# Optimization experiments

Hardware: AMD Instinct MI355X
Metric: run time of the kernel (lower is better)

The kernel has to match this reference:

```python
import jax, jax.numpy as jnp
import numpy as np


def setup_inputs() -> dict:
    key = jax.random.key(0)
    kx, kw = jax.random.split(key)
    x = jax.random.normal(kx, (32, 64, 112, 112), dtype=jnp.float32)
    weights = jax.random.normal(kw, (128, 64, 3, 3), dtype=jnp.float32)
    return {"x": x, "weights": weights}


def reference(x, weights):
    # The torch module's triple loop computes a standard VALID conv2d,
    # stride 1, no padding, weights shared across spatial locations.
    # x: [B, Cin, H, W]; weights: [Cout, Cin, k, k] -> out: [B, Cout, H-k+1, W-k+1]
    out = jax.lax.conv_general_dilated(
        x, weights,
        window_strides=(1, 1),
        padding="VALID",
        dimension_numbers=("NCHW", "OIHW", "NCHW"),
    )
    return out
```

## Files before the change

### kernel.cpp

```cpp
#include <hip/hip_runtime.h>


typedef short bf16x8 __attribute__((ext_vector_type(8)));
typedef float f32x4 __attribute__((ext_vector_type(4)));

__device__ __forceinline__ unsigned short f2bf(float f) {
    unsigned int u = __builtin_bit_cast(unsigned int, f);
    unsigned int r = u + 0x7fffu + ((u >> 16) & 1u);
    return (unsigned short)(r >> 16);
}

__global__ void wperm_kernel(const float* __restrict__ W, unsigned short* __restrict__ wp) {
    int t = blockIdx.x * 256 + threadIdx.x;
    if (t < 73728) {
        int r  = t >> 13;
        int co = (t >> 6) & 127;
        int ci = t & 63;
        wp[t] = f2bf(W[(co * 64 + ci) * 9 + r]);
    }
}

__global__ __launch_bounds__(256, 2) void conv_mfma(const float* __restrict__ x,
                                                    const unsigned short* __restrict__ wp,
                                                    float* __restrict__ out) {
    __shared__ alignas(16) unsigned short xwin[324 * 72];
    __shared__ alignas(16) unsigned short wpl[128 * 72];

    const int tid  = threadIdx.x;
    const int lane = tid & 63;
    const int wv   = tid >> 6;
    const int quad = lane >> 4;
    const int l15  = lane & 15;

    const int b    = blockIdx.x / 49;
    const int tile = blockIdx.x % 49;
    const int oh0  = (tile / 7) * 16;
    const int ow0  = (tile % 7) * 16;

    const float* xb = x + b * 64 * 12544;
    for (int task = tid; task < 288; task += 256) {
        const int cg = task / 18;
        const int hh = task % 18;
        const int h  = min(oh0 + hh, 111);
        const float* xr = xb + (cg * 4) * 12544 + h * 112;
        unsigned short* dst = &xwin[(hh * 18) * 72 + cg * 4];
        #pragma unroll
        for (int ww = 0; ww < 18; ww++) {
            const int w = min(ow0 + ww, 111);
            uint2 v;
            v.x = (unsigned)f2bf(xr[w])         | ((unsigned)f2bf(xr[12544 + w]) << 16);
            v.y = (unsigned)f2bf(xr[25088 + w]) | ((unsigned)f2bf(xr[37632 + w]) << 16);
            *reinterpret_cast<uint2*>(dst + ww * 72) = v;
        }
    }

    f32x4 acc[8][4];
    const f32x4 zero = {0.0f, 0.0f, 0.0f, 0.0f};
    #pragma unroll
    for (int mt = 0; mt < 8; mt++)
        #pragma unroll
        for (int nt = 0; nt < 4; nt++) acc[mt][nt] = zero;

    for (int r = 0; r < 9; r++) {
        const int kh = r / 3;
        const int kw = r % 3;

        __syncthreads();
        {
            const unsigned short* src = wp + r * 8192;
            #pragma unroll
            for (int j = 0; j < 4; j++) {
                const int k   = tid + 256 * j;
                const int co  = k >> 3;
                const int ci0 = (k & 7) * 8;
                uint4 v = *reinterpret_cast<const uint4*>(src + k * 8);
                *reinterpret_cast<uint4*>(&wpl[co * 72 + ci0]) = v;
            }
        }
        __syncthreads();

        #pragma unroll
        for (int cs = 0; cs < 2; cs++) {
            const int ko = cs * 32 + quad * 8;
            bf16x8 bfrag[4];
            #pragma unroll
            for (int nt = 0; nt < 4; nt++) {
                const int t = wv * 4 + nt;
                bfrag[nt] = *reinterpret_cast<const bf16x8*>(
                    &xwin[((t + kh) * 18 + (l15 + kw)) * 72 + ko]);
            }
            #pragma unroll
            for (int mt = 0; mt < 8; mt++) {
                bf16x8 afrag = *reinterpret_cast<const bf16x8*>(
                    &wpl[(mt * 16 + l15) * 72 + ko]);
                #pragma unroll
                for (int nt = 0; nt < 4; nt++)
                    acc[mt][nt] = __builtin_amdgcn_mfma_f32_16x16x32_bf16(
                        afrag, bfrag[nt], acc[mt][nt], 0, 0, 0);
            }
        }
    }

    const int owc = ow0 + l15;
    if (owc < 110) {
        float* ob = out + b * 128 * 12100;
        #pragma unroll
        for (int mt = 0; mt < 8; mt++) {
            #pragma unroll
            for (int nt = 0; nt < 4; nt++) {
                const int oh = oh0 + wv * 4 + nt;
                if (oh < 110) {
                    #pragma unroll
                    for (int reg = 0; reg < 4; reg++) {
                        const int co = mt * 16 + quad * 4 + reg;
                        ob[(co * 110 + oh) * 110 + owc] = acc[mt][nt][reg];
                    }
                }
            }
        }
    }
}

extern "C" void kernel_launch(void* const* d_in, const int* in_sizes, int n_in,
                              void* d_out, int out_size, void* d_ws, size_t ws_size,
                              hipStream_t stream) {
    const float* x = (const float*)d_in[0];
    const float* W = (const float*)d_in[1];
    float* out = (float*)d_out;
    unsigned short* wp = (unsigned short*)d_ws;

    wperm_kernel<<<288, 256, 0, stream>>>(W, wp);
    conv_mfma<<<32 * 49, 256, 0, stream>>>(x, wp, out);
}
```

Baseline: 405.4 us.

## Vectorize input window staging and read weights directly from global memory

The input window is now staged with float4 global loads over channel pairs, and the two halo columns go through a separate clamped loop. This replaces many scalar, poorly coalesced reads. The weight tile is no longer copied into LDS each filter tap; A-fragments are loaded straight from the pre-permuted global buffer, which removes eight barriers per block. Launch bounds are raised to 3 blocks per SM because LDS use drops. The trade-off is repeated global/L2 loads of the weights inside the MFMA loop, plus more register pressure from the higher occupancy target.

After: 529.2 us. 30.5% more time.

```diff
diff --git a/kernel.cpp b/kernel.cpp
--- a/kernel.cpp
+++ b/kernel.cpp
@@ -8,6 +8,9 @@
     unsigned int u = __builtin_bit_cast(unsigned int, f);
     unsigned int r = u + 0x7fffu + ((u >> 16) & 1u);
     return (unsigned short)(r >> 16);
+}
+__device__ __forceinline__ unsigned int pack2(float lo, float hi) {
+    return (unsigned)f2bf(lo) | ((unsigned)f2bf(hi) << 16);
 }
 
 __global__ void wperm_kernel(const float* __restrict__ W, unsigned short* __restrict__ wp) {
@@ -20,11 +23,10 @@
     }
 }
 
-__global__ __launch_bounds__(256, 2) void conv_mfma(const float* __restrict__ x,
+__global__ __launch_bounds__(256, 3) void conv_mfma(const float* __restrict__ x,
                                                     const unsigned short* __restrict__ wp,
                                                     float* __restrict__ out) {
     __shared__ alignas(16) unsigned short xwin[324 * 72];
-    __shared__ alignas(16) unsigned short wpl[128 * 72];
 
     const int tid  = threadIdx.x;
     const int lane = tid & 63;
@@ -37,21 +39,39 @@
     const int oh0  = (tile / 7) * 16;
     const int ow0  = (tile % 7) * 16;
 
-    const float* xb = x + b * 64 * 12544;
-    for (int task = tid; task < 288; task += 256) {
-        const int cg = task / 18;
-        const int hh = task % 18;
-        const int h  = min(oh0 + hh, 111);
-        const float* xr = xb + (cg * 4) * 12544 + h * 112;
-        unsigned short* dst = &xwin[(hh * 18) * 72 + cg * 4];
-        #pragma unroll
-        for (int ww = 0; ww < 18; ww++) {
-            const int w = min(ow0 + ww, 111);
-            uint2 v;
-            v.x = (unsigned)f2bf(xr[w])         | ((unsigned)f2bf(xr[12544 + w]) << 16);
-            v.y = (unsigned)f2bf(xr[25088 + w]) | ((unsigned)f2bf(xr[37632 + w]) << 16);
-            *reinterpret_cast<uint2*>(dst + ww * 72) = v;
-        }
+    const float* xb = x + b * 802816;
+
+    for (int t = tid; t < 2304; t += 256) {
+        const int cgl = t & 7;
+        const int hwl = (t >> 3) & 7;
+        const int cgh = (t >> 6) & 3;
+        const int hwh = t >> 8;
+        const int cg  = cgh * 8 + cgl;
+        const int hw  = hwh * 8 + hwl;
+        const int hh  = hw >> 2;
+        const int wc  = hw & 3;
+        const int h   = min(oh0 + hh, 111);
+        const float* p0 = xb + (2 * cg) * 12544 + h * 112 + ow0 + wc * 4;
+        const f32x4 a = *reinterpret_cast<const f32x4*>(p0);
+        const f32x4 c = *reinterpret_cast<const f32x4*>(p0 + 12544);
+        unsigned int* dst = reinterpret_cast<unsigned int*>(
+            &xwin[(hh * 18 + wc * 4) * 72 + 2 * cg]);
+        dst[0]   = pack2(a[0], c[0]);
+        dst[36]  = pack2(a[1], c[1]);
+        dst[72]  = pack2(a[2], c[2]);
+        dst[108] = pack2(a[3], c[3]);
+    }
+    for (int u = tid; u < 576; u += 256) {
+        const int cg  = u & 31;
+        const int hh  = u >> 5;
+        const int h   = min(oh0 + hh, 111);
+        const int w16 = min(ow0 + 16, 111);
+        const int w17 = min(ow0 + 17, 111);
+        const float* p0 = xb + (2 * cg) * 12544 + h * 112;
+        unsigned int* dst = reinterpret_cast<unsigned int*>(
+            &xwin[(hh * 18 + 16) * 72 + 2 * cg]);
+        dst[0]  = pack2(p0[w16], p0[12544 + w16]);
+        dst[36] = pack2(p0[w17], p0[12544 + w17]);
     }
 
     f32x4 acc[8][4];
@@ -61,38 +81,24 @@
         #pragma unroll
         for (int nt = 0; nt < 4; nt++) acc[mt][nt] = zero;
 
+    __syncthreads();
+
     for (int r = 0; r < 9; r++) {
         const int kh = r / 3;
         const int kw = r % 3;
-
-        __syncthreads();
-        {
-            const unsigned short* src = wp + r * 8192;
-            #pragma unroll
-            for (int j = 0; j < 4; j++) {
-                const int k   = tid + 256 * j;
-                const int co  = k >> 3;
-                const int ci0 = (k & 7) * 8;
-                uint4 v = *reinterpret_cast<const uint4*>(src + k * 8);
-                *reinterpret_cast<uint4*>(&wpl[co * 72 + ci0]) = v;
-            }
-        }
-        __syncthreads();
-
+        const unsigned short* wplane = wp + r * 8192;
         #pragma unroll
         for (int cs = 0; cs < 2; cs++) {
             const int ko = cs * 32 + quad * 8;
             bf16x8 bfrag[4];
             #pragma unroll
-            for (int nt = 0; nt < 4; nt++) {
-                const int t = wv * 4 + nt;
+            for (int nt = 0; nt < 4; nt++)
                 bfrag[nt] = *reinterpret_cast<const bf16x8*>(
-                    &xwin[((t + kh) * 18 + (l15 + kw)) * 72 + ko]);
-            }
+                    &xwin[((wv * 4 + nt + kh) * 18 + (l15 + kw)) * 72 + ko]);
             #pragma unroll
             for (int mt = 0; mt < 8; mt++) {
-                bf16x8 afrag = *reinterpret_cast<const bf16x8*>(
-                    &wpl[(mt * 16 + l15) * 72 + ko]);
+                const bf16x8 afrag = *reinterpret_cast<const bf16x8*>(
+                    wplane + (mt * 16 + l15) * 64 + ko);
                 #pragma unroll
                 for (int nt = 0; nt < 4; nt++)
                     acc[mt][nt] = __builtin_amdgcn_mfma_f32_16x16x32_bf16(
@@ -103,7 +109,7 @@
 
     const int owc = ow0 + l15;
     if (owc < 110) {
-        float* ob = out + b * 128 * 12100;
+        float* ob = out + b * 1548800;
         #pragma unroll
         for (int mt = 0; mt < 8; mt++) {
             #pragma unroll
```
